# Optimization experiments

Measured on AMD Instinct MI355X. Metric: run time of the kernel, lower is better.

## Reference

```python
import jax, jax.numpy as jnp
import numpy as np

NG, CPN, K = 16, 24, 5          # ngroups, channels-per-group, kernel size
C = NG * CPN                     # 384 total channels
PAD = K // 2                     # PseudoEntropyPad(2, ...)


def build_mask():
    """PixelCNN-style group-causal mask for MaskConv2 (hidden/type-B: center
    position allows input group <= output group)."""
    m = np.zeros((C, C, K, K), np.float32)
    m[:, :, :PAD, :] = 1.0                      # rows above center: all allowed
    m[:, :, PAD, :PAD] = 1.0                    # center row, left of center
    g = np.arange(C) // CPN
    m[:, :, PAD, PAD] = (g[None, :] <= g[:, None]).astype(np.float32)
    return jnp.asarray(m)


def masked_conv(x, w, b, mask):
    # zero pad by 2 (PseudoEntropyPad) + VALID 5x5 conv == SAME conv
    y = jax.lax.conv_general_dilated(
        x, w * mask, window_strides=(1, 1), padding=[(PAD, PAD), (PAD, PAD)],
        dimension_numbers=("NCHW", "OIHW", "NCHW"))
    return y + b[None, :, None, None]


def prelu(x, a):
    return jnp.where(x >= 0, x, a[None, :, None, None] * x)


def setup_inputs() -> dict:
    key = jax.random.key(0)
    ks = jax.random.split(key, 5)
    x = jax.random.normal(ks[0], (2, C, 256, 512), dtype=jnp.float32)
    w1 = jax.random.normal(ks[1], (C, C, K, K), dtype=jnp.float32) * 0.02
    w2 = jax.random.normal(ks[2], (C, C, K, K), dtype=jnp.float32) * 0.02
    b1 = jnp.zeros((C,), jnp.float32)
    b2 = jnp.zeros((C,), jnp.float32)
    a1 = jnp.full((C,), 0.25, jnp.float32)   # PReLU init
    a2 = jnp.full((C,), 0.25, jnp.float32)
    return {"x": x, "w1": w1, "b1": b1, "a1": a1, "w2": w2, "b2": b2, "a2": a2}


def reference(x, w1, b1, a1, w2, b2, a2):
    mask = build_mask()
    y = prelu(masked_conv(x, w1, b1, mask), a1)   # EntropyConv 1 (pad+conv+PReLU+trim)
    y = prelu(masked_conv(y, w2, b2, mask), a2)   # EntropyConv 2
    return y + x                                   # residual
```

## Files before the change

### kernel.cpp

```cpp
#include <hip/hip_runtime.h>
#include <hip/hip_bf16.h>


#define C_CH 384
#define HH   256
#define WWD  512
#define NN   2
#define NKC  24
#define PR   260
#define PC   516
#define ICS16 (PR * PC * 16)
#define TCOLS 144
#define PLANE_SH (4 * TCOLS * 16)
#define TSH (2 * PLANE_SH)

typedef __attribute__((ext_vector_type(8)))  short short8;
typedef __attribute__((ext_vector_type(16))) float f32x16;
typedef __attribute__((ext_vector_type(4)))  int   int4v;

typedef const __attribute__((address_space(1))) void* gas_t;
typedef __attribute__((address_space(3))) void* las_t;

__device__ inline unsigned short f2bf(float f) {
    union { float f; unsigned int u; } v; v.f = f;
    unsigned int r = v.u + 0x7FFFu + ((v.u >> 16) & 1u);
    return (unsigned short)(r >> 16);
}

__global__ __launch_bounds__(256) void k_prepack(const float* __restrict__ w1, const float* __restrict__ w2,
                                                 unsigned short* __restrict__ wp1, unsigned short* __restrict__ wp2) {
    int idx = blockIdx.x * 256 + threadIdx.x;
    const int TOT = 13 * NKC * C_CH * 16;
    if (idx >= TOT) return;
    int iq = idx & 15;
    int o  = (idx >> 4) % C_CH;
    int kc = (idx / (16 * C_CH)) % NKC;
    int t  = idx / (16 * C_CH * NKC);
    int i  = kc * 16 + iq;
    int kh = t < 5 ? 0 : (t < 10 ? 1 : 2);
    int kw = t < 5 ? t : (t < 10 ? t - 5 : t - 10);
    bool keep = (t != 12) || ((i / 24) <= (o / 24));
    int src = ((o * C_CH + i) * 5 + kh) * 5 + kw;
    wp1[idx] = keep ? f2bf(w1[src]) : (unsigned short)0;
    wp2[idx] = keep ? f2bf(w2[src]) : (unsigned short)0;
}

__global__ __launch_bounds__(256) void k_repack_x(const float* __restrict__ x, unsigned short* __restrict__ xc) {
    int bid = blockIdx.x;
    int w0 = (bid & 7) << 6;
    int h  = (bid >> 3) & 255;
    int n  = bid >> 11;
    int wi = threadIdx.x & 63;
    int cq = threadIdx.x >> 6;
    int w  = w0 + wi;
    int inb = n * C_CH * HH * WWD + h * WWD + w;
    for (int cc = 0; cc < 12; ++cc) {
        int c0 = cc * 32 + cq * 8;
        short8 outv;
        #pragma unroll
        for (int k = 0; k < 8; ++k) {
            float f = x[inb + (c0 + k) * (HH * WWD)];
            outv[k] = (short)f2bf(f);
        }
        int kc = cc * 2 + (cq >> 1);
        int oidx = (n * NKC + kc) * ICS16 + ((h + 2) * PC + (w + 2)) * 16 + (cq & 1) * 8;
        *(short8*)&xc[oidx] = outv;
    }
}

template<int SECOND>
__global__ __launch_bounds__(256, 2) void k_conv(const unsigned short* __restrict__ in,
                                                 const unsigned short* __restrict__ wp,
                                                 const float* __restrict__ bias,
                                                 const float* __restrict__ alpha,
                                                 const float* __restrict__ xres,
                                                 void* __restrict__ outp) {
    __shared__ __align__(16) unsigned short Xs[2][TSH];

    int bid0 = blockIdx.x;
    int xcd = bid0 & 7;
    int j0  = bid0 >> 3;
    int tile = xcd * 128 + j0 / 3;
    int ob   = j0 % 3;
    int n    = tile >> 9;
    int hp   = (tile >> 2) & 127;
    int wseg = tile & 3;
    int w0 = wseg << 7, o0 = ob << 7, h0 = hp << 1;

    int tid = threadIdx.x;
    int lane = tid & 63;
    int wv = tid >> 6;
    int wr = wv >> 1, wc = wv & 1;
    int lo5 = lane & 31, hi = lane >> 5;

    int goff[9];
    #pragma unroll
    for (int it = 0; it < 9; ++it) {
        int k = wv * 9 + it;
        int plane = k / 18;
        int s = (k % 18) * 64 + lane;
        int r = s / 288;
        int rem = s - r * 288;
        int col = rem >> 1, h16 = rem & 1;
        goff[it] = plane * ICS16 + ((h0 + r) * PC + (w0 + col)) * 16 + h16 * 8;
    }

    const int KH[13] = {0,0,0,0,0,1,1,1,1,1,2,2,2};
    const int KW[13] = {0,1,2,3,4,0,1,2,3,4,0,1,2};

    f32x16 acc[4][2];
    #pragma unroll
    for (int pt = 0; pt < 4; ++pt)
        #pragma unroll
        for (int ot = 0; ot < 2; ++ot)
            #pragma unroll
            for (int r = 0; r < 16; ++r) acc[pt][ot][r] = 0.f;

    const unsigned short* gbase_n = in + (size_t)n * NKC * ICS16;

    #pragma unroll
    for (int it = 0; it < 9; ++it) {
        const unsigned short* gp = gbase_n + goff[it];
        unsigned short* lp = &Xs[0][(wv * 9 + it) * 512];
        __builtin_amdgcn_global_load_lds((gas_t)gp, (las_t)lp, 16, 0, 0);
    }
    __syncthreads();

#define LOAD_XA(dst, u) do {                                              \
        int t_ = (u) >> 1, hf_ = (u) & 1;                                 \
        int so_ = hf_ * PLANE_SH + (wr + KH[t_]) * (TCOLS * 16)           \
                + (lo5 + KW[t_]) * 16 + hi * 8;                           \
        _Pragma("unroll")                                                 \
        for (int pt_ = 0; pt_ < 4; ++pt_)                                 \
            (dst)[pt_] = *(const short8*)&xs[so_ + pt_ * 512];            \
    } while (0)

#define LOAD_WB(dst, u) do {                                              \
        int t_ = (u) >> 1, hf_ = (u) & 1;                                 \
        const unsigned short* wb_ = wp +                                  \
            (size_t)((t_ * NKC + ic * 2 + hf_) * C_CH + o0 + wc * 64) * 16; \
        _Pragma("unroll")                                                 \
        for (int ot_ = 0; ot_ < 2; ++ot_)                                 \
            (dst)[ot_] = *(const short8*)&wb_[(ot_ * 32 + lo5) * 16 + hi * 8]; \
    } while (0)

    for (int ic = 0; ic < 12; ++ic) {
        int buf = ic & 1;
        const unsigned short* xs = &Xs[buf][0];
        if (ic < 11) {
            const unsigned short* gb = gbase_n + (size_t)(ic + 1) * 2 * ICS16;
            #pragma unroll
            for (int it = 0; it < 9; ++it) {
                const unsigned short* gp = gb + goff[it];
                unsigned short* lp = &Xs[buf ^ 1][(wv * 9 + it) * 512];
                __builtin_amdgcn_global_load_lds((gas_t)gp, (las_t)lp, 16, 0, 0);
            }
        }

        short8 xa[2][4];
        short8 wb[3][2];
        LOAD_XA(xa[0], 0);
        LOAD_WB(wb[0], 0);
        LOAD_WB(wb[1], 1);

        #pragma unroll
        for (int s2 = 0; s2 < 26; ++s2) {
            if (s2 + 2 < 26) LOAD_WB(wb[(s2 + 2) % 3], s2 + 2);
            if (s2 + 1 < 26) LOAD_XA(xa[(s2 + 1) & 1], s2 + 1);
            __builtin_amdgcn_s_setprio(1);
            #pragma unroll
            for (int pt = 0; pt < 4; ++pt)
                #pragma unroll
                for (int ot = 0; ot < 2; ++ot) {
                    if (SECOND)
                        acc[pt][ot] = __builtin_amdgcn_mfma_f32_32x32x16_bf16(
                            wb[s2 % 3][ot], xa[s2 & 1][pt], acc[pt][ot], 0, 0, 0);
                    else
                        acc[pt][ot] = __builtin_amdgcn_mfma_f32_32x32x16_bf16(
                            xa[s2 & 1][pt], wb[s2 % 3][ot], acc[pt][ot], 0, 0, 0);
                }
            __builtin_amdgcn_s_setprio(0);
        }
        __syncthreads();
    }
#undef LOAD_XA
#undef LOAD_WB

    int h = h0 + wr;
    if (!SECOND) {
        unsigned short* y = (unsigned short*)outp;
        #pragma unroll
        for (int ot = 0; ot < 2; ++ot) {
            int o = o0 + wc * 64 + ot * 32 + lo5;
            float bo = bias[o], ao = alpha[o];
            int kc = o >> 4;
            int o15 = o & 15;
            size_t base = (size_t)(n * NKC + kc) * ICS16 + ((h + 2) * PC + (w0 + 2)) * 16 + o15;
            #pragma unroll
            for (int pt = 0; pt < 4; ++pt) {
                #pragma unroll
                for (int reg = 0; reg < 16; ++reg) {
                    int p = pt * 32 + (reg & 3) + 8 * (reg >> 2) + 4 * hi;
                    float v = acc[pt][ot][reg] + bo;
                    v = v >= 0.f ? v : ao * v;
                    y[base + (size_t)p * 16] = f2bf(v);
                }
            }
        }
    } else {
        float* outf = (float*)outp;
        #pragma unroll
        for (int ot = 0; ot < 2; ++ot) {
            #pragma unroll
            for (int reg = 0; reg < 16; ++reg) {
                int o = o0 + wc * 64 + ot * 32 + (reg & 3) + 8 * (reg >> 2) + 4 * hi;
                float bo = bias[o], ao = alpha[o];
                #pragma unroll
                for (int pt = 0; pt < 4; ++pt) {
                    int w = w0 + pt * 32 + lo5;
                    float v = acc[pt][ot][reg] + bo;
                    v = v >= 0.f ? v : ao * v;
                    size_t idx = (size_t)((n * C_CH + o) * HH + h) * WWD + w;
                    outf[idx] = v + xres[idx];
                }
            }
        }
    }
}

extern "C" void kernel_launch(void* const* d_in, const int* in_sizes, int n_in,
                              void* d_out, int out_size, void* d_ws, size_t ws_size,
                              hipStream_t stream) {
    const float* x  = (const float*)d_in[0];
    const float* w1 = (const float*)d_in[1];
    const float* b1 = (const float*)d_in[2];
    const float* a1 = (const float*)d_in[3];
    const float* w2 = (const float*)d_in[4];
    const float* b2 = (const float*)d_in[5];
    const float* a2 = (const float*)d_in[6];

    const size_t PLANE_SHORTS = (size_t)NN * NKC * ICS16;
    unsigned short* xc  = (unsigned short*)d_out;
    unsigned short* yb  = (unsigned short*)d_ws;
    unsigned short* wp1 = yb + PLANE_SHORTS;
    unsigned short* wp2 = wp1 + 13 * NKC * C_CH * 16;

    hipMemsetAsync(xc, 0, PLANE_SHORTS * 2, stream);
    hipMemsetAsync(yb, 0, PLANE_SHORTS * 2, stream);

    k_prepack<<<(13 * NKC * C_CH * 16 + 255) / 256, 256, 0, stream>>>(w1, w2, wp1, wp2);
    k_repack_x<<<NN * HH * (WWD / 64), 256, 0, stream>>>(x, xc);
    k_conv<0><<<3072, 256, 0, stream>>>(xc, wp1, b1, a1, nullptr, (void*)yb);
    k_conv<1><<<3072, 256, 0, stream>>>(yb, wp2, b2, a2, x, (void*)d_out);
}
```

Baseline: 1.922 ms.

## Halve conv spatial tile width, raise occupancy, zero only halo borders

The conv kernel's spatial tile shrinks from 128 to 64 output columns per block, so the grid doubles to 6144 blocks. The accumulator count halves and the launch bound asks for 3 blocks per CU, which raises occupancy. The two full-buffer memsets are replaced by a small kernel that zeroes only the padding rows and columns, cutting memory traffic. The cost is more halo re-fetch per output and less weight reuse per block, since each weight fragment now feeds only 2 MFMAs per wave instead of 4.

```diff
diff --git a/kernel.cpp b/kernel.cpp
--- a/kernel.cpp
+++ b/kernel.cpp
@@ -10,13 +10,12 @@
 #define PR   260
 #define PC   516
 #define ICS16 (PR * PC * 16)
-#define TCOLS 144
-#define PLANE_SH (4 * TCOLS * 16)
-#define TSH (2 * PLANE_SH)
+#define TC   80
+#define HFSH (4 * TC * 16)
+#define TSH  (2 * HFSH)
 
 typedef __attribute__((ext_vector_type(8)))  short short8;
 typedef __attribute__((ext_vector_type(16))) float f32x16;
-typedef __attribute__((ext_vector_type(4)))  int   int4v;
 
 typedef const __attribute__((address_space(1))) void* gas_t;
 typedef __attribute__((address_space(3))) void* las_t;
@@ -45,6 +44,27 @@
     wp2[idx] = keep ? f2bf(w2[src]) : (unsigned short)0;
 }
 
+__global__ __launch_bounds__(256) void k_zero_halo(unsigned short* __restrict__ a, unsigned short* __restrict__ b) {
+    int plane = blockIdx.x;
+    const short8 z = (short8){0,0,0,0,0,0,0,0};
+    for (int bi = 0; bi < 2; ++bi) {
+        unsigned short* p = (bi ? b : a) + (size_t)plane * ICS16;
+        for (int i = threadIdx.x; i < 4128; i += 256) {
+            int r4 = i / 1032;
+            int rem = i - r4 * 1032;
+            int row = r4 < 2 ? r4 : 254 + r4;
+            *(short8*)&p[row * (PC * 16) + rem * 8] = z;
+        }
+        for (int i = threadIdx.x; i < 2048; i += 256) {
+            int row = 2 + (i >> 3);
+            int j = i & 7;
+            int col = (j < 4) ? (j >> 1) : (512 + (j >> 1));
+            int q = j & 1;
+            *(short8*)&p[(row * PC + col) * 16 + q * 8] = z;
+        }
+    }
+}
+
 __global__ __launch_bounds__(256) void k_repack_x(const float* __restrict__ x, unsigned short* __restrict__ xc) {
     int bid = blockIdx.x;
     int w0 = (bid & 7) << 6;
@@ -69,7 +89,7 @@
 }
 
 template<int SECOND>
-__global__ __launch_bounds__(256, 2) void k_conv(const unsigned short* __restrict__ in,
+__global__ __launch_bounds__(256, 3) void k_conv(const unsigned short* __restrict__ in,
                                                  const unsigned short* __restrict__ wp,
                                                  const float* __restrict__ bias,
                                                  const float* __restrict__ alpha,
@@ -80,12 +100,12 @@
     int bid0 = blockIdx.x;
     int xcd = bid0 & 7;
     int j0  = bid0 >> 3;
-    int tile = xcd * 128 + j0 / 3;
+    int tile = xcd * 256 + j0 / 3;
     int ob   = j0 % 3;
-    int n    = tile >> 9;
-    int hp   = (tile >> 2) & 127;
-    int wseg = tile & 3;
-    int w0 = wseg << 7, o0 = ob << 7, h0 = hp << 1;
+    int wseg = tile & 7;
+    int hp   = (tile >> 3) & 127;
+    int n    = tile >> 10;
+    int w0 = wseg << 6, o0 = ob << 7, h0 = hp << 1;
 
     int tid = threadIdx.x;
     int lane = tid & 63;
@@ -93,24 +113,25 @@
     int wr = wv >> 1, wc = wv & 1;
     int lo5 = lane & 31, hi = lane >> 5;
 
-    int goff[9];
+    int goff[5];
     #pragma unroll
-    for (int it = 0; it < 9; ++it) {
-        int k = wv * 9 + it;
-        int plane = k / 18;
-        int s = (k % 18) * 64 + lane;
-        int r = s / 288;
-        int rem = s - r * 288;
-        int col = rem >> 1, h16 = rem & 1;
-        goff[it] = plane * ICS16 + ((h0 + r) * PC + (w0 + col)) * 16 + h16 * 8;
+    for (int it = 0; it < 5; ++it) {
+        int k = wv * 5 + it;
+        int s = k * 64 + lane;
+        int hf = s / 640;
+        int rem = s - hf * 640;
+        int row = rem / 160;
+        int rem2 = rem - row * 160;
+        int col = rem2 >> 1, q = rem2 & 1;
+        goff[it] = hf * ICS16 + ((h0 + row) * PC + (w0 + col)) * 16 + q * 8;
     }
 
     const int KH[13] = {0,0,0,0,0,1,1,1,1,1,2,2,2};
     const int KW[13] = {0,1,2,3,4,0,1,2,3,4,0,1,2};
 
-    f32x16 acc[4][2];
+    f32x16 acc[2][2];
     #pragma unroll
-    for (int pt = 0; pt < 4; ++pt)
+    for (int pt = 0; pt < 2; ++pt)
         #pragma unroll
         for (int ot = 0; ot < 2; ++ot)
             #pragma unroll
@@ -119,49 +140,42 @@
     const unsigned short* gbase_n = in + (size_t)n * NKC * ICS16;
 
     #pragma unroll
-    for (int it = 0; it < 9; ++it) {
-        const unsigned short* gp = gbase_n + goff[it];
-        unsigned short* lp = &Xs[0][(wv * 9 + it) * 512];
-        __builtin_amdgcn_global_load_lds((gas_t)gp, (las_t)lp, 16, 0, 0);
-    }
+    for (int it = 0; it < 5; ++it)
+        __builtin_amdgcn_global_load_lds((gas_t)(gbase_n + goff[it]),
+                                         (las_t)&Xs[0][(wv * 5 + it) * 512], 16, 0, 0);
     __syncthreads();
 
 #define LOAD_XA(dst, u) do {                                              \
         int t_ = (u) >> 1, hf_ = (u) & 1;                                 \
-        int so_ = hf_ * PLANE_SH + (wr + KH[t_]) * (TCOLS * 16)           \
+        int so_ = hf_ * HFSH + (wr + KH[t_]) * (TC * 16)                  \
                 + (lo5 + KW[t_]) * 16 + hi * 8;                           \
-        _Pragma("unroll")                                                 \
-        for (int pt_ = 0; pt_ < 4; ++pt_)                                 \
-            (dst)[pt_] = *(const short8*)&xs[so_ + pt_ * 512];            \
+        (dst)[0] = *(const short8*)&xs[so_];                              \
+        (dst)[1] = *(const short8*)&xs[so_ + 512];                        \
     } while (0)
 
 #define LOAD_WB(dst, u) do {                                              \
         int t_ = (u) >> 1, hf_ = (u) & 1;                                 \
         const unsigned short* wb_ = wp +                                  \
             (size_t)((t_ * NKC + ic * 2 + hf_) * C_CH + o0 + wc * 64) * 16; \
-        _Pragma("unroll")                                                 \
-        for (int ot_ = 0; ot_ < 2; ++ot_)                                 \
-            (dst)[ot_] = *(const short8*)&wb_[(ot_ * 32 + lo5) * 16 + hi * 8]; \
+        (dst)[0] = *(const short8*)&wb_[lo5 * 16 + hi * 8];               \
+        (dst)[1] = *(const short8*)&wb_[(32 + lo5) * 16 + hi * 8];        \
     } while (0)
 
     for (int ic = 0; ic < 12; ++ic) {
         int buf = ic & 1;
         const unsigned short* xs = &Xs[buf][0];
+        short8 xa[2][2];
+        short8 wb[3][2];
+        LOAD_WB(wb[0], 0);
+        LOAD_WB(wb[1], 1);
         if (ic < 11) {
             const unsigned short* gb = gbase_n + (size_t)(ic + 1) * 2 * ICS16;
             #pragma unroll
-            for (int it = 0; it < 9; ++it) {
-                const unsigned short* gp = gb + goff[it];
-                unsigned short* lp = &Xs[buf ^ 1][(wv * 9 + it) * 512];
-                __builtin_amdgcn_global_load_lds((gas_t)gp, (las_t)lp, 16, 0, 0);
-            }
-        }
-
-        short8 xa[2][4];
-        short8 wb[3][2];
+            for (int it = 0; it < 5; ++it)
+                __builtin_amdgcn_global_load_lds((gas_t)(gb + goff[it]),
+                                                 (las_t)&Xs[buf ^ 1][(wv * 5 + it) * 512], 16, 0, 0);
+        }
         LOAD_XA(xa[0], 0);
-        LOAD_WB(wb[0], 0);
-        LOAD_WB(wb[1], 1);
 
         #pragma unroll
         for (int s2 = 0; s2 < 26; ++s2) {
@@ -169,7 +183,7 @@
             if (s2 + 1 < 26) LOAD_XA(xa[(s2 + 1) & 1], s2 + 1);
             __builtin_amdgcn_s_setprio(1);
             #pragma unroll
-            for (int pt = 0; pt < 4; ++pt)
+            for (int pt = 0; pt < 2; ++pt)
                 #pragma unroll
                 for (int ot = 0; ot < 2; ++ot) {
                     if (SECOND)
@@ -197,7 +211,7 @@
             int o15 = o & 15;
             size_t base = (size_t)(n * NKC + kc) * ICS16 + ((h + 2) * PC + (w0 + 2)) * 16 + o15;
             #pragma unroll
-            for (int pt = 0; pt < 4; ++pt) {
+            for (int pt = 0; pt < 2; ++pt) {
                 #pragma unroll
                 for (int reg = 0; reg < 16; ++reg) {
                     int p = pt * 32 + (reg & 3) + 8 * (reg >> 2) + 4 * hi;
@@ -216,7 +230,7 @@
                 int o = o0 + wc * 64 + ot * 32 + (reg & 3) + 8 * (reg >> 2) + 4 * hi;
                 float bo = bias[o], ao = alpha[o];
                 #pragma unroll
-                for (int pt = 0; pt < 4; ++pt) {
+                for (int pt = 0; pt < 2; ++pt) {
                     int w = w0 + pt * 32 + lo5;
                     float v = acc[pt][ot][reg] + bo;
                     v = v >= 0.f ? v : ao * v;
@@ -245,11 +259,9 @@
     unsigned short* wp1 = yb + PLANE_SHORTS;
     unsigned short* wp2 = wp1 + 13 * NKC * C_CH * 16;
 
-    hipMemsetAsync(xc, 0, PLANE_SHORTS * 2, stream);
-    hipMemsetAsync(yb, 0, PLANE_SHORTS * 2, stream);
-
     k_prepack<<<(13 * NKC * C_CH * 16 + 255) / 256, 256, 0, stream>>>(w1, w2, wp1, wp2);
+    k_zero_halo<<<NN * NKC, 256, 0, stream>>>(xc, yb);
     k_repack_x<<<NN * HH * (WWD / 64), 256, 0, stream>>>(x, xc);
-    k_conv<0><<<3072, 256, 0, stream>>>(xc, wp1, b1, a1, nullptr, (void*)yb);
-    k_conv<1><<<3072, 256, 0, stream>>>(yb, wp2, b2, a2, x, (void*)d_out);
-}
+    k_conv<0><<<6144, 256, 0, stream>>>(xc, wp1, b1, a1, nullptr, (void*)yb);
+    k_conv<1><<<6144, 256, 0, stream>>>(yb, wp2, b2, a2, x, (void*)d_out);
+}
```

New measurement: 2.105 ms. +9.5%, slower.
